# Performance work log

Measured on AMD Instinct MI355X. Metric: run time of the kernel, lower is better.

Reference implementation:

```python
import jax, jax.numpy as jnp
import numpy as np

# ---- reconstructed Constants (repo's Constants module is external) ----
DT, DX, DY, Z = 0.005, 0.01, 0.01, 1.0
_cf = np.array([-11.0 / 6.0, 3.0, -1.5, 1.0 / 3.0], np.float32)  # 3rd-order one-sided stencil
KF  = jnp.asarray(((DT / DX) * _cf).reshape(1, 4, 1, 1))           # H-field forward boundary kernel
KB  = jnp.asarray((-(DT / DX) * _cf[::-1]).reshape(1, 4, 1, 1))    # H-field backward boundary kernel
KEF = jnp.asarray(((DT / (Z * DY)) * _cf).reshape(1, 4, 1, 1))     # E-field forward boundary kernel
KEB = jnp.asarray((-(DT / (Z * DY)) * _cf[::-1]).reshape(1, 4, 1, 1))

PAD1   = ((0, 0), (2, 2), (2, 2), (0, 0))
PAD2   = ((0, 0), (0, 0), (1, 1), (0, 0))
PAD3   = ((0, 0), (1, 1), (0, 0), (0, 0))
PADY_F = ((0, 0), (0, 4), (1, 1), (0, 0))
PADY_B = ((0, 0), (4, 0), (1, 1), (0, 0))
PADX_F = ((0, 0), (1, 1), (0, 4), (0, 0))
PADX_B = ((0, 0), (1, 1), (4, 0), (0, 0))
PADEX_F = ((0, 0), (0, 0), (0, 2), (0, 0))
PADEX_B = ((0, 0), (0, 0), (2, 0), (0, 0))
PADEY_F = ((0, 0), (0, 2), (0, 0), (0, 0))
PADEY_B = ((0, 0), (2, 0), (0, 0), (0, 0))


def _conv(x, k):  # TF-style VALID cross-correlation, NHWC/HWIO
    return jax.lax.conv_general_dilated(x, k, (1, 1), 'VALID',
                                        dimension_numbers=('NHWC', 'HWIO', 'NHWC'))


def _T(k):  # swap the two spatial kernel dims (tf.transpose perm=[1,0,2,3])
    return jnp.transpose(k, (1, 0, 2, 3))


def _amper(E, Hx, Hy, f):
    S1 = (jnp.pad(DT / DX * _conv(Hy, _T(f)), PAD1)
          + jnp.pad(_conv(Hy, _T(KF)), PADY_F)
          + jnp.pad(_conv(Hy, _T(KB)), PADY_B))
    S2 = (jnp.pad(Z * DT / DY * _conv(Hx, f), PAD1)
          + jnp.pad(_conv(Hx, KF), PADX_F)
          + jnp.pad(_conv(Hx, KB), PADX_B))
    return E + S1 - S2


def _faraday(E, Hx, Hy, f):
    S3 = (DT / (Z * DY) * jnp.pad(_conv(E, f), PAD2)
          + jnp.pad(_conv(E, KEF), PADEX_F)[:, 1:-1, :, :]
          + jnp.pad(_conv(E, KEB), PADEX_B)[:, 1:-1, :, :])
    S4 = (DT / (Z * DX) * jnp.pad(_conv(E, _T(f)), PAD3)
          + jnp.pad(_conv(E, _T(KEF)), PADEY_F)[:, :, 1:-1, :]
          + jnp.pad(_conv(E, _T(KEB)), PADEY_B)[:, :, 1:-1, :])
    return Hx - S3, Hy + S4


def setup_inputs() -> dict:
    key = jax.random.key(0)
    k1, k2, k3 = jax.random.split(key, 3)
    B, P, Q = 8, 1024, 1024
    E = jax.random.normal(k1, (B, P, Q, 1), jnp.float32)
    Hx = jax.random.normal(k2, (B, P - 2, Q - 1, 1), jnp.float32)
    Hy = jax.random.normal(k3, (B, P - 1, Q - 2, 1), jnp.float32)
    filt = jnp.array([[1.0, -1.0, 1.0, 0.0],
                      [0.0, -1.0, 1.0, 0.0],
                      [1.0, -1.0, 1.0, 0.0]], jnp.float32).reshape(3, 4, 1, 1)
    return {'E': E, 'Hx': Hx, 'Hy': Hy, 'filt': filt}


def reference(E, Hx, Hy, filt):
    E_n = _amper(E, Hx, Hy, filt)
    Hx_n, Hy_n = _faraday(E_n, Hx, Hy, filt)
    E_m = _amper(E_n, Hx_n, Hy_n, filt)
    Hx_m, Hy_m = _faraday(E_m, Hx_n, Hy_n, filt)
    return (jnp.concatenate([E_n, E_m], 1),
            jnp.concatenate([Hx_n, Hx_m], 1),
            jnp.concatenate([Hy_n, Hy_m], 1))
```

## Files before the change

kernel.cpp:

```cpp
#include <hip/hip_runtime.h>


#define KF0 (-11.0f / 12.0f)
#define KF1 (1.5f)
#define KF2 (-0.75f)
#define KF3 (1.0f / 6.0f)
#define KB0 (-1.0f / 6.0f)
#define KB1 (0.75f)
#define KB2 (-1.5f)
#define KB3 (11.0f / 12.0f)

typedef float f4 __attribute__((ext_vector_type(4)));
typedef float f2 __attribute__((ext_vector_type(2)));

__device__ __forceinline__ f4 ld4(const float* p) { f4 v; __builtin_memcpy(&v, p, 16); return v; }
__device__ __forceinline__ f2 ld2(const float* p) { f2 v; __builtin_memcpy(&v, p, 8); return v; }
__device__ __forceinline__ void st4(float* p, f4 v) { __builtin_memcpy(p, &v, 16); }

#define LOAD6(dst, p) do { f4 _a = ld4(p); f2 _b = ld2((p) + 4); \
    (dst)[0]=_a.x; (dst)[1]=_a.y; (dst)[2]=_a.z; (dst)[3]=_a.w; (dst)[4]=_b.x; (dst)[5]=_b.y; } while (0)
#define LOAD4(dst, p) do { f4 _a = ld4(p); \
    (dst)[0]=_a.x; (dst)[1]=_a.y; (dst)[2]=_a.z; (dst)[3]=_a.w; } while (0)


__device__ __forceinline__ float amper_pt(const float* __restrict__ e,
                                          const float* __restrict__ hx,
                                          const float* __restrict__ hy,
                                          int y, int x)
{
    float v = e[y * 1024 + x];
    if ((y >= 2) & (y < 1022) & (x >= 2) & (x < 1022)) {
        const float* r0 = hy + (y - 2) * 1022 + (x - 2);
        const float* r1 = r0 + 1022;
        const float* r2 = r1 + 1022;
        v += 0.5f * ((r0[0] + r0[2])
                     - (r1[0] + r1[1] + r1[2])
                     + (r2[0] + r2[1] + r2[2]));
        const float* q0 = hx + (y - 2) * 1023 + (x - 2);
        const float* q1 = q0 + 1023;
        const float* q2 = q1 + 1023;
        v -= 0.5f * ((q0[0] - q0[1] + q0[2])
                     + (-q1[1] + q1[2])
                     + (q2[0] - q2[1] + q2[2]));
    }
    bool cx = (x >= 1) & (x < 1023);
    if ((y < 1020) & cx) {
        const float* c = hy + y * 1022 + (x - 1);
        v += KF0 * c[0] + KF1 * c[1022] + KF2 * c[2044] + KF3 * c[3066];
    }
    if ((y >= 4) & cx) {
        const float* c = hy + (y - 4) * 1022 + (x - 1);
        v += KB0 * c[0] + KB1 * c[1022] + KB2 * c[2044] + KB3 * c[3066];
    }
    bool cy = (y >= 1) & (y < 1023);
    if (cy & (x < 1020)) {
        const float* r = hx + (y - 1) * 1023 + x;
        v -= KF0 * r[0] + KF1 * r[1] + KF2 * r[2] + KF3 * r[3];
    }
    if (cy & (x >= 4)) {
        const float* r = hx + (y - 1) * 1023 + (x - 4);
        v -= KB0 * r[0] + KB1 * r[1] + KB2 * r[2] + KB3 * r[3];
    }
    return v;
}

__device__ __forceinline__ float far_hx_pt(const float* __restrict__ e,
                                           const float* __restrict__ hxp,
                                           int y, int x)
{
    float v = hxp[y * 1023 + x];
    if ((x >= 1) & (x < 1022)) {
        const float* r0 = e + y * 1024 + (x - 1);
        const float* r1 = r0 + 1024;
        const float* r2 = r1 + 1024;
        v -= 0.5f * ((r0[0] - r0[1] + r0[2])
                     + (-r1[1] + r1[2])
                     + (r2[0] - r2[1] + r2[2]));
    }
    if (x < 1021) {
        const float* r = e + (y + 1) * 1024 + x;
        v -= KF0 * r[0] + KF1 * r[1] + KF2 * r[2] + KF3 * r[3];
    }
    if (x >= 2) {
        const float* r = e + (y + 1) * 1024 + (x - 2);
        v -= KB0 * r[0] + KB1 * r[1] + KB2 * r[2] + KB3 * r[3];
    }
    return v;
}

__device__ __forceinline__ float far_hy_pt(const float* __restrict__ e,
                                           const float* __restrict__ hyp,
                                           int y, int x)
{
    float v = hyp[y * 1022 + x];
    if ((y >= 1) & (y < 1022)) {
        const float* r0 = e + (y - 1) * 1024 + x;
        const float* r1 = r0 + 1024;
        const float* r2 = r1 + 1024;
        v += 0.5f * ((r0[0] + r0[2])
                     - (r1[0] + r1[1] + r1[2])
                     + (r2[0] + r2[1] + r2[2]));
    }
    if (y < 1021) {
        const float* c = e + y * 1024 + (x + 1);
        v += KF0 * c[0] + KF1 * c[1024] + KF2 * c[2048] + KF3 * c[3072];
    }
    if (y >= 2) {
        const float* c = e + (y - 2) * 1024 + (x + 1);
        v += KB0 * c[0] + KB1 * c[1024] + KB2 * c[2048] + KB3 * c[3072];
    }
    return v;
}


__global__ __launch_bounds__(256) void amper_k(
    const float* __restrict__ E, int sEb,
    const float* __restrict__ Hx, int sHxb,
    const float* __restrict__ Hy, int sHyb,
    float* __restrict__ Eo, int sEob)
{
    int lin = blockIdx.y + (blockIdx.z << 10);
    int b = lin & 7;
    int y = lin >> 3;
    int x0 = threadIdx.x << 2;

    const float* e  = E  + (size_t)b * sEb;
    const float* hx = Hx + (size_t)b * sHxb;
    const float* hy = Hy + (size_t)b * sHyb;
    float* eo = Eo + (size_t)b * sEob + y * 1024;

    if ((y >= 4) & (y < 1020) & (x0 >= 4) & (x0 <= 1016)) {
        float cA[6], cB[6], cC[6];
        const float* hyr = hy + (y - 2) * 1022 + (x0 - 2);
        LOAD6(cA, hyr);
        LOAD6(cB, hyr + 1022);
        LOAD6(cC, hyr + 2044);
        float km4[4], km3[4], kp1[4], kp2[4], kp3[4];
        const float* hyc = hy + (y - 4) * 1022 + (x0 - 1);
        LOAD4(km4, hyc);
        LOAD4(km3, hyc + 1022);
        LOAD4(kp1, hyc + 5 * 1022);
        LOAD4(kp2, hyc + 6 * 1022);
        LOAD4(kp3, hyc + 7 * 1022);
        float dA[6], dC[6], e12[12];
        const float* hxr = hx + (y - 2) * 1023 + (x0 - 2);
        LOAD6(dA, hxr);
        LOAD6(dC, hxr + 2046);
        const float* hxm = hx + (y - 1) * 1023 + (x0 - 4);
        LOAD4(&e12[0], hxm);
        LOAD4(&e12[4], hxm + 4);
        LOAD4(&e12[8], hxm + 8);
        f4 ev = ld4(e + y * 1024 + x0);
        f4 o;
        #pragma unroll
        for (int j = 0; j < 4; ++j) {
            float v = ev[j];
            v += 0.5f * ((cA[j] + cA[j + 2])
                         - (cB[j] + cB[j + 1] + cB[j + 2])
                         + (cC[j] + cC[j + 1] + cC[j + 2]));
            v -= 0.5f * ((dA[j] - dA[j + 1] + dA[j + 2])
                         + (-e12[j + 3] + e12[j + 4])
                         + (dC[j] - dC[j + 1] + dC[j + 2]));
            v += KF0 * cC[j + 1] + KF1 * kp1[j] + KF2 * kp2[j] + KF3 * kp3[j];
            v += KB0 * km4[j] + KB1 * km3[j] + KB2 * cA[j + 1] + KB3 * cB[j + 1];
            v -= KF0 * e12[j + 4] + KF1 * e12[j + 5] + KF2 * e12[j + 6] + KF3 * e12[j + 7];
            v -= KB0 * e12[j] + KB1 * e12[j + 1] + KB2 * e12[j + 2] + KB3 * e12[j + 3];
            o[j] = v;
        }
        st4(eo + x0, o);
    } else {
        #pragma unroll
        for (int j = 0; j < 4; ++j)
            eo[x0 + j] = amper_pt(e, hx, hy, y, x0 + j);
    }
}


__global__ __launch_bounds__(256) void faraday_k(
    const float* __restrict__ E, int sEb,
    const float* __restrict__ Hx, int sHxb,
    const float* __restrict__ Hy, int sHyb,
    float* __restrict__ Hxo, int sHxob,
    float* __restrict__ Hyo, int sHyob)
{
    int lin = blockIdx.y + 1023 * blockIdx.z;
    int b = lin & 7;
    int y = lin >> 3;
    int x0 = threadIdx.x << 2;

    const float* e = E + (size_t)b * sEb;
    bool xfast = (x0 >= 4) & (x0 <= 1016);

    if (y < 1022) {
        const float* hxp = Hx + (size_t)b * sHxb;
        float* hxo = Hxo + (size_t)b * sHxob + y * 1023;
        if (xfast) {
            float gA[6], gC[6], h9[9];
            const float* er = e + y * 1024 + (x0 - 1);
            LOAD6(gA, er);
            LOAD6(gC, er + 2048);
            const float* em = e + (y + 1) * 1024 + (x0 - 2);
            LOAD4(&h9[0], em);
            LOAD4(&h9[4], em + 4);
            h9[8] = em[8];
            f4 hv = ld4(hxp + y * 1023 + x0);
            f4 o;
            #pragma unroll
            for (int j = 0; j < 4; ++j) {
                float v = hv[j];
                v -= 0.5f * ((gA[j] - gA[j + 1] + gA[j + 2])
                             + (-h9[j + 2] + h9[j + 3])
                             + (gC[j] - gC[j + 1] + gC[j + 2]));
                v -= KF0 * h9[j + 2] + KF1 * h9[j + 3] + KF2 * h9[j + 4] + KF3 * h9[j + 5];
                v -= KB0 * h9[j] + KB1 * h9[j + 1] + KB2 * h9[j + 2] + KB3 * h9[j + 3];
                o[j] = v;
            }
            st4(hxo + x0, o);
        } else {
            for (int j = 0; j < 4; ++j) {
                int x = x0 + j;
                if (x < 1023) hxo[x] = far_hx_pt(e, hxp, y, x);
            }
        }
    }

    {
        const float* hyp = Hy + (size_t)b * sHyb;
        float* hyo = Hyo + (size_t)b * sHyob + y * 1022;
        if (xfast & (y >= 2) & (y <= 1020)) {
            float mA[6], mB[6], mC[6], nA[4], nD[4], nE[4];
            const float* er = e + (y - 1) * 1024 + x0;
            LOAD6(mA, er);
            LOAD6(mB, er + 1024);
            LOAD6(mC, er + 2048);
            const float* en = e + (y - 2) * 1024 + (x0 + 1);
            LOAD4(nA, en);
            LOAD4(nD, en + 4 * 1024);
            LOAD4(nE, en + 5 * 1024);
            f4 hv = ld4(hyp + y * 1022 + x0);
            f4 o;
            #pragma unroll
            for (int j = 0; j < 4; ++j) {
                float v = hv[j];
                v += 0.5f * ((mA[j] + mA[j + 2])
                             - (mB[j] + mB[j + 1] + mB[j + 2])
                             + (mC[j] + mC[j + 1] + mC[j + 2]));
                v += KF0 * mB[j + 1] + KF1 * mC[j + 1] + KF2 * nD[j] + KF3 * nE[j];
                v += KB0 * nA[j] + KB1 * mA[j + 1] + KB2 * mB[j + 1] + KB3 * mC[j + 1];
                o[j] = v;
            }
            st4(hyo + x0, o);
        } else {
            for (int j = 0; j < 4; ++j) {
                int x = x0 + j;
                if (x < 1022) hyo[x] = far_hy_pt(e, hyp, y, x);
            }
        }
    }
}

extern "C" void kernel_launch(void* const* d_in, const int* in_sizes, int n_in,
                              void* d_out, int out_size, void* d_ws, size_t ws_size,
                              hipStream_t stream)
{
    const float* E  = (const float*)d_in[0];
    const float* Hx = (const float*)d_in[1];
    const float* Hy = (const float*)d_in[2];

    float* out = (float*)d_out;
    float* Eo  = out;
    float* Hxo = out + 16777216;
    float* Hyo = Hxo + 16728096;

    const int sE = 1024 * 1024;
    const int sHx = 1022 * 1023;
    const int sHy = 1023 * 1022;
    const int sEo = 2 * 1024 * 1024;
    const int sHo = 2 * 1045506;

    dim3 blk(256, 1, 1);
    dim3 gA(1, 1024, 8);
    dim3 gF(1, 1023, 8);

    amper_k<<<gA, blk, 0, stream>>>(E, sE, Hx, sHx, Hy, sHy, Eo, sEo);
    faraday_k<<<gF, blk, 0, stream>>>(Eo, sEo, Hx, sHx, Hy, sHy,
                                      Hxo, sHo, Hyo, sHo);
    amper_k<<<gA, blk, 0, stream>>>(Eo, sEo, Hxo, sHo, Hyo, sHo,
                                    Eo + 1024 * 1024, sEo);
    faraday_k<<<gF, blk, 0, stream>>>(Eo + 1024 * 1024, sEo, Hxo, sHo, Hyo, sHo,
                                      Hxo + 1045506, sHo, Hyo + 1045506, sHo);
}
```

Before: 400.5 us.

## Fuse four stencil passes into one cooperative kernel with grid syncs

```diff
diff --git a/kernel.cpp b/kernel.cpp
--- a/kernel.cpp
+++ b/kernel.cpp
@@ -1,4 +1,7 @@
 #include <hip/hip_runtime.h>
+#include <hip/hip_cooperative_groups.h>
+
+namespace cg = cooperative_groups;
 
 
 #define KF0 (-11.0f / 12.0f)
@@ -113,21 +116,12 @@
 }
 
 
-__global__ __launch_bounds__(256) void amper_k(
-    const float* __restrict__ E, int sEb,
-    const float* __restrict__ Hx, int sHxb,
-    const float* __restrict__ Hy, int sHyb,
-    float* __restrict__ Eo, int sEob)
-{
-    int lin = blockIdx.y + (blockIdx.z << 10);
-    int b = lin & 7;
-    int y = lin >> 3;
-    int x0 = threadIdx.x << 2;
-
-    const float* e  = E  + (size_t)b * sEb;
-    const float* hx = Hx + (size_t)b * sHxb;
-    const float* hy = Hy + (size_t)b * sHyb;
-    float* eo = Eo + (size_t)b * sEob + y * 1024;
+__device__ __forceinline__ void amper_row(
+    const float* __restrict__ e, const float* __restrict__ hx,
+    const float* __restrict__ hy, float* __restrict__ eoB, int y, int tid)
+{
+    int x0 = tid << 2;
+    float* eo = eoB + y * 1024;
 
     if ((y >= 4) & (y < 1020) & (x0 >= 4) & (x0 <= 1016)) {
         float cA[6], cB[6], cC[6];
@@ -175,25 +169,16 @@
     }
 }
 
-
-__global__ __launch_bounds__(256) void faraday_k(
-    const float* __restrict__ E, int sEb,
-    const float* __restrict__ Hx, int sHxb,
-    const float* __restrict__ Hy, int sHyb,
-    float* __restrict__ Hxo, int sHxob,
-    float* __restrict__ Hyo, int sHyob)
-{
-    int lin = blockIdx.y + 1023 * blockIdx.z;
-    int b = lin & 7;
-    int y = lin >> 3;
-    int x0 = threadIdx.x << 2;
-
-    const float* e = E + (size_t)b * sEb;
+__device__ __forceinline__ void faraday_row(
+    const float* __restrict__ e, const float* __restrict__ hxp,
+    const float* __restrict__ hyp, float* __restrict__ hxoB,
+    float* __restrict__ hyoB, int y, int tid)
+{
+    int x0 = tid << 2;
     bool xfast = (x0 >= 4) & (x0 <= 1016);
 
     if (y < 1022) {
-        const float* hxp = Hx + (size_t)b * sHxb;
-        float* hxo = Hxo + (size_t)b * sHxob + y * 1023;
+        float* hxo = hxoB + y * 1023;
         if (xfast) {
             float gA[6], gC[6], h9[9];
             const float* er = e + y * 1024 + (x0 - 1);
@@ -225,8 +210,7 @@
     }
 
     {
-        const float* hyp = Hy + (size_t)b * sHyb;
-        float* hyo = Hyo + (size_t)b * sHyob + y * 1022;
+        float* hyo = hyoB + y * 1022;
         if (xfast & (y >= 2) & (y <= 1020)) {
             float mA[6], mB[6], mC[6], nA[4], nD[4], nE[4];
             const float* er = e + (y - 1) * 1024 + x0;
@@ -259,6 +243,85 @@
     }
 }
 
+
+__global__ __launch_bounds__(256, 4) void fdtd_fused(
+    const float* __restrict__ E, const float* __restrict__ Hx,
+    const float* __restrict__ Hy, float* __restrict__ Eo,
+    float* __restrict__ Hxo, float* __restrict__ Hyo)
+{
+    int tid = threadIdx.x;
+    int blk = blockIdx.x;
+    int b = blk & 7;
+    int ys = (blk >> 3) << 3;
+
+    const float* e  = E  + (size_t)b * (1024 * 1024);
+    const float* hx = Hx + (size_t)b * (1022 * 1023);
+    const float* hy = Hy + (size_t)b * (1023 * 1022);
+    float* eo1  = Eo  + (size_t)b * (2 * 1024 * 1024);
+    float* eo2  = eo1 + 1024 * 1024;
+    float* hxo1 = Hxo + (size_t)b * (2 * 1045506);
+    float* hxo2 = hxo1 + 1045506;
+    float* hyo1 = Hyo + (size_t)b * (2 * 1045506);
+    float* hyo2 = hyo1 + 1045506;
+
+    cg::grid_group grid = cg::this_grid();
+
+    #pragma unroll 1
+    for (int i = 0; i < 8; ++i)
+        amper_row(e, hx, hy, eo1, ys + i, tid);
+    __threadfence();
+    grid.sync();
+
+    #pragma unroll 1
+    for (int i = 0; i < 8; ++i) {
+        int y = ys + i;
+        if (y < 1023) faraday_row(eo1, hx, hy, hxo1, hyo1, y, tid);
+    }
+    __threadfence();
+    grid.sync();
+
+    #pragma unroll 1
+    for (int i = 0; i < 8; ++i)
+        amper_row(eo1, hxo1, hyo1, eo2, ys + i, tid);
+    __threadfence();
+    grid.sync();
+
+    #pragma unroll 1
+    for (int i = 0; i < 8; ++i) {
+        int y = ys + i;
+        if (y < 1023) faraday_row(eo2, hxo1, hyo1, hxo2, hyo2, y, tid);
+    }
+}
+
+
+__global__ __launch_bounds__(256) void amper_k(
+    const float* __restrict__ E, int sEb,
+    const float* __restrict__ Hx, int sHxb,
+    const float* __restrict__ Hy, int sHyb,
+    float* __restrict__ Eo, int sEob)
+{
+    int lin = blockIdx.y + (blockIdx.z << 10);
+    int b = lin & 7;
+    int y = lin >> 3;
+    amper_row(E + (size_t)b * sEb, Hx + (size_t)b * sHxb,
+              Hy + (size_t)b * sHyb, Eo + (size_t)b * sEob, y, threadIdx.x);
+}
+
+__global__ __launch_bounds__(256) void faraday_k(
+    const float* __restrict__ E, int sEb,
+    const float* __restrict__ Hx, int sHxb,
+    const float* __restrict__ Hy, int sHyb,
+    float* __restrict__ Hxo, int sHxob,
+    float* __restrict__ Hyo, int sHyob)
+{
+    int lin = blockIdx.y + 1023 * blockIdx.z;
+    int b = lin & 7;
+    int y = lin >> 3;
+    faraday_row(E + (size_t)b * sEb, Hx + (size_t)b * sHxb,
+                Hy + (size_t)b * sHyb, Hxo + (size_t)b * sHxob,
+                Hyo + (size_t)b * sHyob, y, threadIdx.x);
+}
+
 extern "C" void kernel_launch(void* const* d_in, const int* in_sizes, int n_in,
                               void* d_out, int out_size, void* d_ws, size_t ws_size,
                               hipStream_t stream)
@@ -272,21 +335,27 @@
     float* Hxo = out + 16777216;
     float* Hyo = Hxo + 16728096;
 
-    const int sE = 1024 * 1024;
-    const int sHx = 1022 * 1023;
-    const int sHy = 1023 * 1022;
-    const int sEo = 2 * 1024 * 1024;
-    const int sHo = 2 * 1045506;
-
-    dim3 blk(256, 1, 1);
-    dim3 gA(1, 1024, 8);
-    dim3 gF(1, 1023, 8);
-
-    amper_k<<<gA, blk, 0, stream>>>(E, sE, Hx, sHx, Hy, sHy, Eo, sEo);
-    faraday_k<<<gF, blk, 0, stream>>>(Eo, sEo, Hx, sHx, Hy, sHy,
-                                      Hxo, sHo, Hyo, sHo);
-    amper_k<<<gA, blk, 0, stream>>>(Eo, sEo, Hxo, sHo, Hyo, sHo,
-                                    Eo + 1024 * 1024, sEo);
-    faraday_k<<<gF, blk, 0, stream>>>(Eo + 1024 * 1024, sEo, Hxo, sHo, Hyo, sHo,
-                                      Hxo + 1045506, sHo, Hyo + 1045506, sHo);
-}
+    void* kargs[6] = { (void*)&E, (void*)&Hx, (void*)&Hy,
+                       (void*)&Eo, (void*)&Hxo, (void*)&Hyo };
+    hipError_t err = hipLaunchCooperativeKernel(
+        reinterpret_cast<void*>(fdtd_fused),
+        dim3(1024, 1, 1), dim3(256, 1, 1), kargs, 0, stream);
+
+    if (err != hipSuccess) {
+        const int sE = 1024 * 1024;
+        const int sHx = 1022 * 1023;
+        const int sHy = 1023 * 1022;
+        const int sEo = 2 * 1024 * 1024;
+        const int sHo = 2 * 1045506;
+        dim3 blk(256, 1, 1);
+        dim3 gA(1, 1024, 8);
+        dim3 gF(1, 1023, 8);
+        amper_k<<<gA, blk, 0, stream>>>(E, sE, Hx, sHx, Hy, sHy, Eo, sEo);
+        faraday_k<<<gF, blk, 0, stream>>>(Eo, sEo, Hx, sHx, Hy, sHy,
+                                          Hxo, sHo, Hyo, sHo);
+        amper_k<<<gA, blk, 0, stream>>>(Eo, sEo, Hxo, sHo, Hyo, sHo,
+                                        Eo + 1024 * 1024, sEo);
+        faraday_k<<<gF, blk, 0, stream>>>(Eo + 1024 * 1024, sEo, Hxo, sHo, Hyo, sHo,
+                                          Hxo + 1045506, sHo, Hyo + 1045506, sHo);
+    }
+}
```

Result: slower. 1.318 ms (+229.1%).

## Stage H and E stencil halos in LDS with 4-row by 512-column block tiles

Applied to the files above, without the earlier changes.

```diff
diff --git a/kernel.cpp b/kernel.cpp
--- a/kernel.cpp
+++ b/kernel.cpp
@@ -14,104 +14,49 @@
 typedef float f2 __attribute__((ext_vector_type(2)));
 
 __device__ __forceinline__ f4 ld4(const float* p) { f4 v; __builtin_memcpy(&v, p, 16); return v; }
-__device__ __forceinline__ f2 ld2(const float* p) { f2 v; __builtin_memcpy(&v, p, 8); return v; }
 __device__ __forceinline__ void st4(float* p, f4 v) { __builtin_memcpy(p, &v, 16); }
 
-#define LOAD6(dst, p) do { f4 _a = ld4(p); f2 _b = ld2((p) + 4); \
-    (dst)[0]=_a.x; (dst)[1]=_a.y; (dst)[2]=_a.z; (dst)[3]=_a.w; (dst)[4]=_b.x; (dst)[5]=_b.y; } while (0)
-#define LOAD4(dst, p) do { f4 _a = ld4(p); \
-    (dst)[0]=_a.x; (dst)[1]=_a.y; (dst)[2]=_a.z; (dst)[3]=_a.w; } while (0)
-
-
-__device__ __forceinline__ float amper_pt(const float* __restrict__ e,
-                                          const float* __restrict__ hx,
-                                          const float* __restrict__ hy,
-                                          int y, int x)
+#define LOAD6(dst, p) do { __builtin_memcpy(dst, p, 24); } while (0)
+#define LOAD4(dst, p) do { __builtin_memcpy(dst, p, 16); } while (0)
+
+
+#define HYP 520
+#define HYS_AT(r, c) hyS[((r) - y0 + 4) * HYP + ((c) - xb + 4)]
+#define HXS_AT(r, c) hxS[((r) - y0 + 2) * HYP + ((c) - xb + 4)]
+
+__device__ __forceinline__ float amper_pt_lds(
+    const float* __restrict__ e, const float* hxS, const float* hyS,
+    int y0, int xb, int y, int x)
 {
     float v = e[y * 1024 + x];
     if ((y >= 2) & (y < 1022) & (x >= 2) & (x < 1022)) {
-        const float* r0 = hy + (y - 2) * 1022 + (x - 2);
-        const float* r1 = r0 + 1022;
-        const float* r2 = r1 + 1022;
-        v += 0.5f * ((r0[0] + r0[2])
-                     - (r1[0] + r1[1] + r1[2])
-                     + (r2[0] + r2[1] + r2[2]));
-        const float* q0 = hx + (y - 2) * 1023 + (x - 2);
-        const float* q1 = q0 + 1023;
-        const float* q2 = q1 + 1023;
-        v -= 0.5f * ((q0[0] - q0[1] + q0[2])
-                     + (-q1[1] + q1[2])
-                     + (q2[0] - q2[1] + q2[2]));
+        v += 0.5f * ((HYS_AT(y-2, x-2) + HYS_AT(y-2, x))
+                     - (HYS_AT(y-1, x-2) + HYS_AT(y-1, x-1) + HYS_AT(y-1, x))
+                     + (HYS_AT(y, x-2) + HYS_AT(y, x-1) + HYS_AT(y, x)));
+        v -= 0.5f * ((HXS_AT(y-2, x-2) - HXS_AT(y-2, x-1) + HXS_AT(y-2, x))
+                     + (-HXS_AT(y-1, x-1) + HXS_AT(y-1, x))
+                     + (HXS_AT(y, x-2) - HXS_AT(y, x-1) + HXS_AT(y, x)));
     }
     bool cx = (x >= 1) & (x < 1023);
     if ((y < 1020) & cx) {
-        const float* c = hy + y * 1022 + (x - 1);
-        v += KF0 * c[0] + KF1 * c[1022] + KF2 * c[2044] + KF3 * c[3066];
+        v += KF0 * HYS_AT(y, x-1) + KF1 * HYS_AT(y+1, x-1)
+           + KF2 * HYS_AT(y+2, x-1) + KF3 * HYS_AT(y+3, x-1);
     }
     if ((y >= 4) & cx) {
-        const float* c = hy + (y - 4) * 1022 + (x - 1);
-        v += KB0 * c[0] + KB1 * c[1022] + KB2 * c[2044] + KB3 * c[3066];
+        v += KB0 * HYS_AT(y-4, x-1) + KB1 * HYS_AT(y-3, x-1)
+           + KB2 * HYS_AT(y-2, x-1) + KB3 * HYS_AT(y-1, x-1);
     }
     bool cy = (y >= 1) & (y < 1023);
     if (cy & (x < 1020)) {
-        const float* r = hx + (y - 1) * 1023 + x;
-        v -= KF0 * r[0] + KF1 * r[1] + KF2 * r[2] + KF3 * r[3];
+        v -= KF0 * HXS_AT(y-1, x) + KF1 * HXS_AT(y-1, x+1)
+           + KF2 * HXS_AT(y-1, x+2) + KF3 * HXS_AT(y-1, x+3);
     }
     if (cy & (x >= 4)) {
-        const float* r = hx + (y - 1) * 1023 + (x - 4);
-        v -= KB0 * r[0] + KB1 * r[1] + KB2 * r[2] + KB3 * r[3];
+        v -= KB0 * HXS_AT(y-1, x-4) + KB1 * HXS_AT(y-1, x-3)
+           + KB2 * HXS_AT(y-1, x-2) + KB3 * HXS_AT(y-1, x-1);
     }
     return v;
 }
-
-__device__ __forceinline__ float far_hx_pt(const float* __restrict__ e,
-                                           const float* __restrict__ hxp,
-                                           int y, int x)
-{
-    float v = hxp[y * 1023 + x];
-    if ((x >= 1) & (x < 1022)) {
-        const float* r0 = e + y * 1024 + (x - 1);
-        const float* r1 = r0 + 1024;
-        const float* r2 = r1 + 1024;
-        v -= 0.5f * ((r0[0] - r0[1] + r0[2])
-                     + (-r1[1] + r1[2])
-                     + (r2[0] - r2[1] + r2[2]));
-    }
-    if (x < 1021) {
-        const float* r = e + (y + 1) * 1024 + x;
-        v -= KF0 * r[0] + KF1 * r[1] + KF2 * r[2] + KF3 * r[3];
-    }
-    if (x >= 2) {
-        const float* r = e + (y + 1) * 1024 + (x - 2);
-        v -= KB0 * r[0] + KB1 * r[1] + KB2 * r[2] + KB3 * r[3];
-    }
-    return v;
-}
-
-__device__ __forceinline__ float far_hy_pt(const float* __restrict__ e,
-                                           const float* __restrict__ hyp,
-                                           int y, int x)
-{
-    float v = hyp[y * 1022 + x];
-    if ((y >= 1) & (y < 1022)) {
-        const float* r0 = e + (y - 1) * 1024 + x;
-        const float* r1 = r0 + 1024;
-        const float* r2 = r1 + 1024;
-        v += 0.5f * ((r0[0] + r0[2])
-                     - (r1[0] + r1[1] + r1[2])
-                     + (r2[0] + r2[1] + r2[2]));
-    }
-    if (y < 1021) {
-        const float* c = e + y * 1024 + (x + 1);
-        v += KF0 * c[0] + KF1 * c[1024] + KF2 * c[2048] + KF3 * c[3072];
-    }
-    if (y >= 2) {
-        const float* c = e + (y - 2) * 1024 + (x + 1);
-        v += KB0 * c[0] + KB1 * c[1024] + KB2 * c[2048] + KB3 * c[3072];
-    }
-    return v;
-}
-
 
 __global__ __launch_bounds__(256) void amper_k(
     const float* __restrict__ E, int sEb,
@@ -119,62 +64,159 @@
     const float* __restrict__ Hy, int sHyb,
     float* __restrict__ Eo, int sEob)
 {
-    int lin = blockIdx.y + (blockIdx.z << 10);
-    int b = lin & 7;
-    int y = lin >> 3;
-    int x0 = threadIdx.x << 2;
+    int xt = blockIdx.x;
+    int b  = blockIdx.y;
+    int s  = blockIdx.z;
+    int y0 = s << 2;
+    int xb = xt << 9;
 
     const float* e  = E  + (size_t)b * sEb;
     const float* hx = Hx + (size_t)b * sHxb;
     const float* hy = Hy + (size_t)b * sHyb;
-    float* eo = Eo + (size_t)b * sEob + y * 1024;
-
-    if ((y >= 4) & (y < 1020) & (x0 >= 4) & (x0 <= 1016)) {
-        float cA[6], cB[6], cC[6];
-        const float* hyr = hy + (y - 2) * 1022 + (x0 - 2);
-        LOAD6(cA, hyr);
-        LOAD6(cB, hyr + 1022);
-        LOAD6(cC, hyr + 2044);
-        float km4[4], km3[4], kp1[4], kp2[4], kp3[4];
-        const float* hyc = hy + (y - 4) * 1022 + (x0 - 1);
-        LOAD4(km4, hyc);
-        LOAD4(km3, hyc + 1022);
-        LOAD4(kp1, hyc + 5 * 1022);
-        LOAD4(kp2, hyc + 6 * 1022);
-        LOAD4(kp3, hyc + 7 * 1022);
-        float dA[6], dC[6], e12[12];
-        const float* hxr = hx + (y - 2) * 1023 + (x0 - 2);
-        LOAD6(dA, hxr);
-        LOAD6(dC, hxr + 2046);
-        const float* hxm = hx + (y - 1) * 1023 + (x0 - 4);
-        LOAD4(&e12[0], hxm);
-        LOAD4(&e12[4], hxm + 4);
-        LOAD4(&e12[8], hxm + 8);
-        f4 ev = ld4(e + y * 1024 + x0);
-        f4 o;
-        #pragma unroll
-        for (int j = 0; j < 4; ++j) {
-            float v = ev[j];
-            v += 0.5f * ((cA[j] + cA[j + 2])
-                         - (cB[j] + cB[j + 1] + cB[j + 2])
-                         + (cC[j] + cC[j + 1] + cC[j + 2]));
-            v -= 0.5f * ((dA[j] - dA[j + 1] + dA[j + 2])
-                         + (-e12[j + 3] + e12[j + 4])
-                         + (dC[j] - dC[j + 1] + dC[j + 2]));
-            v += KF0 * cC[j + 1] + KF1 * kp1[j] + KF2 * kp2[j] + KF3 * kp3[j];
-            v += KB0 * km4[j] + KB1 * km3[j] + KB2 * cA[j + 1] + KB3 * cB[j + 1];
-            v -= KF0 * e12[j + 4] + KF1 * e12[j + 5] + KF2 * e12[j + 6] + KF3 * e12[j + 7];
-            v -= KB0 * e12[j] + KB1 * e12[j + 1] + KB2 * e12[j + 2] + KB3 * e12[j + 3];
-            o[j] = v;
-        }
-        st4(eo + x0, o);
-    } else {
-        #pragma unroll
-        for (int j = 0; j < 4; ++j)
-            eo[x0 + j] = amper_pt(e, hx, hy, y, x0 + j);
-    }
-}
-
+    float* eo = Eo + (size_t)b * sEob;
+
+    __shared__ float hyS[11 * HYP];
+    __shared__ float hxS[6 * HYP];
+
+    int tid = threadIdx.x;
+
+    for (int idx = tid; idx < 11 * 130; idx += 256) {
+        int i = idx / 130, j = idx - i * 130;
+        int gr = y0 - 4 + i;
+        int gc = xb - 4 + (j << 2);
+        f4 v = {0.f, 0.f, 0.f, 0.f};
+        if ((unsigned)gr < 1023u) {
+            const float* p = hy + gr * 1022;
+            if ((gc >= 0) & (gc + 3 < 1022)) v = ld4(p + gc);
+            else {
+                #pragma unroll
+                for (int k = 0; k < 4; ++k) {
+                    int c = gc + k;
+                    if ((unsigned)c < 1022u) v[k] = p[c];
+                }
+            }
+        }
+        st4(&hyS[i * HYP + (j << 2)], v);
+    }
+    for (int idx = tid; idx < 6 * 130; idx += 256) {
+        int i = idx / 130, j = idx - i * 130;
+        int gr = y0 - 2 + i;
+        int gc = xb - 4 + (j << 2);
+        f4 v = {0.f, 0.f, 0.f, 0.f};
+        if ((unsigned)gr < 1022u) {
+            const float* p = hx + gr * 1023;
+            if ((gc >= 0) & (gc + 3 < 1023)) v = ld4(p + gc);
+            else {
+                #pragma unroll
+                for (int k = 0; k < 4; ++k) {
+                    int c = gc + k;
+                    if ((unsigned)c < 1023u) v[k] = p[c];
+                }
+            }
+        }
+        st4(&hxS[i * HYP + (j << 2)], v);
+    }
+    __syncthreads();
+
+    int tx = tid & 127, ty = tid >> 7;
+    int c0 = xb + (tx << 2);
+
+    #pragma unroll
+    for (int rr = 0; rr < 2; ++rr) {
+        int y = y0 + (ty << 1) + rr;
+        float* eorow = eo + y * 1024;
+        if ((y >= 4) & (y < 1020) & (c0 >= 4) & (c0 <= 1016)) {
+            const float* hyr = &hyS[(y - y0 + 2) * HYP + (c0 - xb + 2)];
+            float cA[6], cB[6], cC[6];
+            LOAD6(cA, hyr);
+            LOAD6(cB, hyr + HYP);
+            LOAD6(cC, hyr + 2 * HYP);
+            const float* hyc = &hyS[(y - y0) * HYP + (c0 - xb + 3)];
+            float km4[4], km3[4], kp1[4], kp2[4], kp3[4];
+            LOAD4(km4, hyc);
+            LOAD4(km3, hyc + HYP);
+            LOAD4(kp1, hyc + 5 * HYP);
+            LOAD4(kp2, hyc + 6 * HYP);
+            LOAD4(kp3, hyc + 7 * HYP);
+            const float* hxr = &hxS[(y - y0) * HYP + (c0 - xb + 2)];
+            float dA[6], dC[6], e12[12];
+            LOAD6(dA, hxr);
+            LOAD6(dC, hxr + 2 * HYP);
+            const float* hxm = &hxS[(y - y0 + 1) * HYP + (c0 - xb)];
+            LOAD4(&e12[0], hxm);
+            LOAD4(&e12[4], hxm + 4);
+            LOAD4(&e12[8], hxm + 8);
+            f4 ev = ld4(e + y * 1024 + c0);
+            f4 o;
+            #pragma unroll
+            for (int j = 0; j < 4; ++j) {
+                float v = ev[j];
+                v += 0.5f * ((cA[j] + cA[j + 2])
+                             - (cB[j] + cB[j + 1] + cB[j + 2])
+                             + (cC[j] + cC[j + 1] + cC[j + 2]));
+                v -= 0.5f * ((dA[j] - dA[j + 1] + dA[j + 2])
+                             + (-e12[j + 3] + e12[j + 4])
+                             + (dC[j] - dC[j + 1] + dC[j + 2]));
+                v += KF0 * cC[j + 1] + KF1 * kp1[j] + KF2 * kp2[j] + KF3 * kp3[j];
+                v += KB0 * km4[j] + KB1 * km3[j] + KB2 * cA[j + 1] + KB3 * cB[j + 1];
+                v -= KF0 * e12[j + 4] + KF1 * e12[j + 5] + KF2 * e12[j + 6] + KF3 * e12[j + 7];
+                v -= KB0 * e12[j] + KB1 * e12[j + 1] + KB2 * e12[j + 2] + KB3 * e12[j + 3];
+                o[j] = v;
+            }
+            st4(eorow + c0, o);
+        } else {
+            #pragma unroll
+            for (int j = 0; j < 4; ++j)
+                eorow[c0 + j] = amper_pt_lds(e, hxS, hyS, y0, xb, y, c0 + j);
+        }
+    }
+}
+
+
+#define EP 524
+#define ES_AT(r, c) eS[((r) - y0 + 2) * EP + ((c) - xb + 4)]
+
+__device__ __forceinline__ float far_hx_pt_lds(
+    const float* eS, const float* __restrict__ hxp,
+    int y0, int xb, int y, int x)
+{
+    float v = hxp[y * 1023 + x];
+    if ((x >= 1) & (x < 1022)) {
+        v -= 0.5f * ((ES_AT(y, x-1) - ES_AT(y, x) + ES_AT(y, x+1))
+                     + (-ES_AT(y+1, x) + ES_AT(y+1, x+1))
+                     + (ES_AT(y+2, x-1) - ES_AT(y+2, x) + ES_AT(y+2, x+1)));
+    }
+    if (x < 1021) {
+        v -= KF0 * ES_AT(y+1, x) + KF1 * ES_AT(y+1, x+1)
+           + KF2 * ES_AT(y+1, x+2) + KF3 * ES_AT(y+1, x+3);
+    }
+    if (x >= 2) {
+        v -= KB0 * ES_AT(y+1, x-2) + KB1 * ES_AT(y+1, x-1)
+           + KB2 * ES_AT(y+1, x) + KB3 * ES_AT(y+1, x+1);
+    }
+    return v;
+}
+
+__device__ __forceinline__ float far_hy_pt_lds(
+    const float* eS, const float* __restrict__ hyp,
+    int y0, int xb, int y, int x)
+{
+    float v = hyp[y * 1022 + x];
+    if ((y >= 1) & (y < 1022)) {
+        v += 0.5f * ((ES_AT(y-1, x) + ES_AT(y-1, x+2))
+                     - (ES_AT(y, x) + ES_AT(y, x+1) + ES_AT(y, x+2))
+                     + (ES_AT(y+1, x) + ES_AT(y+1, x+1) + ES_AT(y+1, x+2)));
+    }
+    if (y < 1021) {
+        v += KF0 * ES_AT(y, x+1) + KF1 * ES_AT(y+1, x+1)
+           + KF2 * ES_AT(y+2, x+1) + KF3 * ES_AT(y+3, x+1);
+    }
+    if (y >= 2) {
+        v += KB0 * ES_AT(y-2, x+1) + KB1 * ES_AT(y-1, x+1)
+           + KB2 * ES_AT(y, x+1) + KB3 * ES_AT(y+1, x+1);
+    }
+    return v;
+}
 
 __global__ __launch_bounds__(256) void faraday_k(
     const float* __restrict__ E, int sEb,
@@ -183,77 +225,114 @@
     float* __restrict__ Hxo, int sHxob,
     float* __restrict__ Hyo, int sHyob)
 {
-    int lin = blockIdx.y + 1023 * blockIdx.z;
-    int b = lin & 7;
-    int y = lin >> 3;
-    int x0 = threadIdx.x << 2;
-
-    const float* e = E + (size_t)b * sEb;
-    bool xfast = (x0 >= 4) & (x0 <= 1016);
-
-    if (y < 1022) {
-        const float* hxp = Hx + (size_t)b * sHxb;
-        float* hxo = Hxo + (size_t)b * sHxob + y * 1023;
-        if (xfast) {
-            float gA[6], gC[6], h9[9];
-            const float* er = e + y * 1024 + (x0 - 1);
-            LOAD6(gA, er);
-            LOAD6(gC, er + 2048);
-            const float* em = e + (y + 1) * 1024 + (x0 - 2);
-            LOAD4(&h9[0], em);
-            LOAD4(&h9[4], em + 4);
-            h9[8] = em[8];
-            f4 hv = ld4(hxp + y * 1023 + x0);
-            f4 o;
-            #pragma unroll
-            for (int j = 0; j < 4; ++j) {
-                float v = hv[j];
-                v -= 0.5f * ((gA[j] - gA[j + 1] + gA[j + 2])
-                             + (-h9[j + 2] + h9[j + 3])
-                             + (gC[j] - gC[j + 1] + gC[j + 2]));
-                v -= KF0 * h9[j + 2] + KF1 * h9[j + 3] + KF2 * h9[j + 4] + KF3 * h9[j + 5];
-                v -= KB0 * h9[j] + KB1 * h9[j + 1] + KB2 * h9[j + 2] + KB3 * h9[j + 3];
-                o[j] = v;
-            }
-            st4(hxo + x0, o);
-        } else {
-            for (int j = 0; j < 4; ++j) {
-                int x = x0 + j;
-                if (x < 1023) hxo[x] = far_hx_pt(e, hxp, y, x);
-            }
-        }
-    }
-
-    {
-        const float* hyp = Hy + (size_t)b * sHyb;
-        float* hyo = Hyo + (size_t)b * sHyob + y * 1022;
-        if (xfast & (y >= 2) & (y <= 1020)) {
-            float mA[6], mB[6], mC[6], nA[4], nD[4], nE[4];
-            const float* er = e + (y - 1) * 1024 + x0;
-            LOAD6(mA, er);
-            LOAD6(mB, er + 1024);
-            LOAD6(mC, er + 2048);
-            const float* en = e + (y - 2) * 1024 + (x0 + 1);
-            LOAD4(nA, en);
-            LOAD4(nD, en + 4 * 1024);
-            LOAD4(nE, en + 5 * 1024);
-            f4 hv = ld4(hyp + y * 1022 + x0);
-            f4 o;
-            #pragma unroll
-            for (int j = 0; j < 4; ++j) {
-                float v = hv[j];
-                v += 0.5f * ((mA[j] + mA[j + 2])
-                             - (mB[j] + mB[j + 1] + mB[j + 2])
-                             + (mC[j] + mC[j + 1] + mC[j + 2]));
-                v += KF0 * mB[j + 1] + KF1 * mC[j + 1] + KF2 * nD[j] + KF3 * nE[j];
-                v += KB0 * nA[j] + KB1 * mA[j + 1] + KB2 * mB[j + 1] + KB3 * mC[j + 1];
-                o[j] = v;
-            }
-            st4(hyo + x0, o);
-        } else {
-            for (int j = 0; j < 4; ++j) {
-                int x = x0 + j;
-                if (x < 1022) hyo[x] = far_hy_pt(e, hyp, y, x);
+    int xt = blockIdx.x;
+    int b  = blockIdx.y;
+    int s  = blockIdx.z;
+    int y0 = s << 2;
+    int xb = xt << 9;
+
+    const float* e   = E  + (size_t)b * sEb;
+    const float* hxp = Hx + (size_t)b * sHxb;
+    const float* hyp = Hy + (size_t)b * sHyb;
+    float* hxo = Hxo + (size_t)b * sHxob;
+    float* hyo = Hyo + (size_t)b * sHyob;
+
+    __shared__ float eS[9 * EP];
+
+    int tid = threadIdx.x;
+
+    for (int idx = tid; idx < 9 * 131; idx += 256) {
+        int i = idx / 131, j = idx - i * 131;
+        int gr = y0 - 2 + i;
+        int gc = xb - 4 + (j << 2);
+        f4 v = {0.f, 0.f, 0.f, 0.f};
+        if ((unsigned)gr < 1024u) {
+            const float* p = e + gr * 1024;
+            if ((gc >= 0) & (gc + 3 < 1024)) v = ld4(p + gc);
+            else {
+                #pragma unroll
+                for (int k = 0; k < 4; ++k) {
+                    int c = gc + k;
+                    if ((unsigned)c < 1024u) v[k] = p[c];
+                }
+            }
+        }
+        st4(&eS[i * EP + (j << 2)], v);
+    }
+    __syncthreads();
+
+    int tx = tid & 127, ty = tid >> 7;
+    int c0 = xb + (tx << 2);
+    bool cfast = (c0 >= 4) & (c0 <= 1016);
+
+    #pragma unroll
+    for (int rr = 0; rr < 2; ++rr) {
+        int y = y0 + (ty << 1) + rr;
+
+        if (y < 1022) {
+            float* hxorow = hxo + y * 1023;
+            if (cfast) {
+                const float* er = &eS[(y - y0 + 2) * EP + (c0 - xb + 3)];
+                float gA[6], gC[6], h9[9];
+                LOAD6(gA, er);
+                LOAD6(gC, er + 2 * EP);
+                const float* em = &eS[(y - y0 + 3) * EP + (c0 - xb + 2)];
+                LOAD4(&h9[0], em);
+                LOAD4(&h9[4], em + 4);
+                h9[8] = em[8];
+                f4 hv = ld4(hxp + y * 1023 + c0);
+                f4 o;
+                #pragma unroll
+                for (int j = 0; j < 4; ++j) {
+                    float v = hv[j];
+                    v -= 0.5f * ((gA[j] - gA[j + 1] + gA[j + 2])
+                                 + (-h9[j + 2] + h9[j + 3])
+                                 + (gC[j] - gC[j + 1] + gC[j + 2]));
+                    v -= KF0 * h9[j + 2] + KF1 * h9[j + 3] + KF2 * h9[j + 4] + KF3 * h9[j + 5];
+                    v -= KB0 * h9[j] + KB1 * h9[j + 1] + KB2 * h9[j + 2] + KB3 * h9[j + 3];
+                    o[j] = v;
+                }
+                st4(hxorow + c0, o);
+            } else {
+                #pragma unroll
+                for (int j = 0; j < 4; ++j) {
+                    int x = c0 + j;
+                    if (x < 1023) hxorow[x] = far_hx_pt_lds(eS, hxp, y0, xb, y, x);
+                }
+            }
+        }
+
+        if (y < 1023) {
+            float* hyorow = hyo + y * 1022;
+            if (cfast & (y >= 2) & (y <= 1020)) {
+                const float* er = &eS[(y - y0 + 1) * EP + (c0 - xb + 4)];
+                float mA[6], mB[6], mC[6], nA[4], nD[4], nE[4];
+                LOAD6(mA, er);
+                LOAD6(mB, er + EP);
+                LOAD6(mC, er + 2 * EP);
+                const float* en = &eS[(y - y0) * EP + (c0 - xb + 5)];
+                LOAD4(nA, en);
+                LOAD4(nD, en + 4 * EP);
+                LOAD4(nE, en + 5 * EP);
+                f4 hv = ld4(hyp + y * 1022 + c0);
+                f4 o;
+                #pragma unroll
+                for (int j = 0; j < 4; ++j) {
+                    float v = hv[j];
+                    v += 0.5f * ((mA[j] + mA[j + 2])
+                                 - (mB[j] + mB[j + 1] + mB[j + 2])
+                                 + (mC[j] + mC[j + 1] + mC[j + 2]));
+                    v += KF0 * mB[j + 1] + KF1 * mC[j + 1] + KF2 * nD[j] + KF3 * nE[j];
+                    v += KB0 * nA[j] + KB1 * mA[j + 1] + KB2 * mB[j + 1] + KB3 * mC[j + 1];
+                    o[j] = v;
+                }
+                st4(hyorow + c0, o);
+            } else {
+                #pragma unroll
+                for (int j = 0; j < 4; ++j) {
+                    int x = c0 + j;
+                    if (x < 1022) hyorow[x] = far_hy_pt_lds(eS, hyp, y0, xb, y, x);
+                }
             }
         }
     }
@@ -279,14 +358,13 @@
     const int sHo = 2 * 1045506;
 
     dim3 blk(256, 1, 1);
-    dim3 gA(1, 1024, 8);
-    dim3 gF(1, 1023, 8);
-
-    amper_k<<<gA, blk, 0, stream>>>(E, sE, Hx, sHx, Hy, sHy, Eo, sEo);
-    faraday_k<<<gF, blk, 0, stream>>>(Eo, sEo, Hx, sHx, Hy, sHy,
-                                      Hxo, sHo, Hyo, sHo);
-    amper_k<<<gA, blk, 0, stream>>>(Eo, sEo, Hxo, sHo, Hyo, sHo,
-                                    Eo + 1024 * 1024, sEo);
-    faraday_k<<<gF, blk, 0, stream>>>(Eo + 1024 * 1024, sEo, Hxo, sHo, Hyo, sHo,
-                                      Hxo + 1045506, sHo, Hyo + 1045506, sHo);
-}
+    dim3 g(2, 8, 256);
+
+    amper_k<<<g, blk, 0, stream>>>(E, sE, Hx, sHx, Hy, sHy, Eo, sEo);
+    faraday_k<<<g, blk, 0, stream>>>(Eo, sEo, Hx, sHx, Hy, sHy,
+                                     Hxo, sHo, Hyo, sHo);
+    amper_k<<<g, blk, 0, stream>>>(Eo, sEo, Hxo, sHo, Hyo, sHo,
+                                   Eo + 1024 * 1024, sEo);
+    faraday_k<<<g, blk, 0, stream>>>(Eo + 1024 * 1024, sEo, Hxo, sHo, Hyo, sHo,
+                                     Hxo + 1045506, sHo, Hyo + 1045506, sHo);
+}
```

Measured after the change: 416.3 us. +4.0%, slower.
